# Performance work log

Measured on AMD Instinct MI355X. Metric: run time of the kernel, lower is better.

The kernel has to match this reference:

```python
import jax, jax.numpy as jnp
import numpy as np

B, S, D, H, T, MAXLEN = 8, 1024, 768, 12, 384, 1024
HD = D // H  # spatial head dim = 64
SCALE = HD ** -0.5


def setup_inputs() -> dict:
    key = jax.random.key(0)
    ks = jax.random.split(key, 16)

    def lin(k, din, dout):
        kw, _ = jax.random.split(k)
        w = jax.random.normal(kw, (din, dout), jnp.float32) / np.sqrt(din).astype(np.float32)
        b = jnp.zeros((dout,), jnp.float32)
        return w, b

    Wqs, bqs = lin(ks[0], D, D)
    Wks, bks = lin(ks[1], D, D)
    Wvs, bvs = lin(ks[2], D, D)
    Wqt, bqt = lin(ks[3], T, D)
    Wkt, bkt = lin(ks[4], T, D)
    Wvt, bvt = lin(ks[5], T, D)
    Er = jax.random.normal(ks[6], (MAXLEN, HD), jnp.float32)
    patches = jax.random.normal(ks[7], (B, S, D), jnp.float32)
    time_emb = jax.random.normal(ks[8], (B, T), jnp.float32)
    return dict(patches=patches, time_emb=time_emb,
                Wqs=Wqs, bqs=bqs, Wks=Wks, bks=bks, Wvs=Wvs, bvs=bvs,
                Wqt=Wqt, bqt=bqt, Wkt=Wkt, bkt=bkt, Wvt=Wvt, bvt=bvt, Er=Er)


def _skew(QEr):
    # QEr: [B, H, S, S] -> pad one zero col on the left, reshape, drop first row.
    b, h, r, c = QEr.shape
    padded = jnp.pad(QEr, ((0, 0), (0, 0), (0, 0), (1, 0)))  # [B,H,r,c+1]
    reshaped = padded.reshape(b, h, c + 1, r)
    return reshaped[:, :, 1:, :]  # [B,H,S,S]


def reference(patches, time_emb, Wqs, bqs, Wks, bks, Wvs, bvs,
              Wqt, bqt, Wkt, bkt, Wvt, bvt, Er):
    b, s, _ = patches.shape

    def heads(x):  # [B,S,D] -> [B,H,S,HD]
        return x.reshape(b, -1, H, HD).transpose(0, 2, 1, 3)

    qs = heads(patches @ Wqs + bqs)
    ks = heads(patches @ Wks + bks)
    vs = heads(patches @ Wvs + bvs)
    qt = heads(time_emb @ Wqt + bqt)  # [B,H,1,HD]
    kt = heads(time_emb @ Wkt + bkt)
    vt = heads(time_emb @ Wvt + bvt)

    q = qs + qt
    k = ks + kt
    v = vs + vt

    Er_slice = Er[MAXLEN - s:, :]                      # [S, HD]
    QEr = jnp.einsum('bhsd,td->bhst', qs, Er_slice)    # [B,H,S,S]
    Srel = _skew(QEr)

    scores = (jnp.einsum('bhqd,bhkd->bhqk', q, k) + Srel) * SCALE
    attn = jax.nn.softmax(scores, axis=-1)
    out = jnp.einsum('bhqk,bhkd->bhqd', attn, v)       # [B,H,S,HD]
    return out.transpose(0, 2, 1, 3).reshape(b, s, H * HD)
```

## Files before the change

kernel.cpp:

```cpp
#include <hip/hip_runtime.h>

typedef __attribute__((ext_vector_type(8))) short short8;
typedef __attribute__((ext_vector_type(4))) float floatx4;

#define CSC 0.1803368801f

__device__ __forceinline__ unsigned short f2b(float f){
  unsigned int u = __builtin_bit_cast(unsigned int, f);
  unsigned int r = (u + 0x7fffu + ((u >> 16) & 1u)) >> 16;
  return (unsigned short)r;
}
__device__ __forceinline__ float b2f(unsigned short h){
  unsigned int u = ((unsigned int)h) << 16;
  return __builtin_bit_cast(float, u);
}
__device__ __forceinline__ floatx4 mfma16(short8 a, short8 b, floatx4 c){
  return __builtin_amdgcn_mfma_f32_16x16x32_bf16(a, b, c, 0, 0, 0);
}

__global__ __launch_bounds__(256) void transpose_w(
    const float* __restrict__ Wq, const float* __restrict__ Wk,
    const float* __restrict__ Wv, unsigned short* __restrict__ Wb){
  __shared__ float tile[64][65];
  int g = blockIdx.z;
  const float* W = (g==0) ? Wq : (g==1) ? Wk : Wv;
  int r0 = blockIdx.y*64, c0 = blockIdx.x*64;
  int tx = threadIdx.x & 63, ty = threadIdx.x >> 6;
  #pragma unroll
  for (int i=0;i<16;i++){
    int r = i*4 + ty;
    tile[r][tx] = W[(r0+r)*768 + c0 + tx];
  }
  __syncthreads();
  unsigned short* dst = Wb + g*589824;
  #pragma unroll
  for (int i=0;i<16;i++){
    int rr = i*4 + ty;
    dst[(c0+rr)*768 + r0 + tx] = f2b(tile[tx][rr]);
  }
}

__global__ __launch_bounds__(256) void convert_kernel(
    const float* __restrict__ patches, const float* __restrict__ Er,
    const float* __restrict__ temb,
    const float* __restrict__ Wqt, const float* __restrict__ bqt,
    const float* __restrict__ Wkt, const float* __restrict__ bkt,
    const float* __restrict__ Wvt, const float* __restrict__ bvt,
    unsigned short* __restrict__ Pb, unsigned short* __restrict__ Erb,
    float* __restrict__ Tmat){
  int blk = blockIdx.x, tid = threadIdx.x;
  if (blk < 3104){
    const float* src; unsigned short* dst; int idx;
    if (blk < 3072){ idx = blk*2048 + tid*8; src = patches; dst = Pb; }
    else           { idx = (blk-3072)*2048 + tid*8; src = Er; dst = Erb; }
    float4 f0 = *(const float4*)(src + idx);
    float4 f1 = *(const float4*)(src + idx + 4);
    uint4 pk;
    pk.x = (unsigned)f2b(f0.x) | ((unsigned)f2b(f0.y)<<16);
    pk.y = (unsigned)f2b(f0.z) | ((unsigned)f2b(f0.w)<<16);
    pk.z = (unsigned)f2b(f1.x) | ((unsigned)f2b(f1.y)<<16);
    pk.w = (unsigned)f2b(f1.z) | ((unsigned)f2b(f1.w)<<16);
    *(uint4*)(dst + idx) = pk;
  } else {
    int g = (blk-3104)>>3, bb = (blk-3104)&7;
    const float* Wt = (g==0)? Wqt : (g==1)? Wkt : Wvt;
    const float* bt = (g==0)? bqt : (g==1)? bkt : bvt;
    __shared__ float emb[384];
    for (int j=tid;j<384;j+=256) emb[j] = temb[bb*384 + j];
    __syncthreads();
    float acc0 = bt[tid], acc1 = bt[tid+256], acc2 = bt[tid+512];
    for (int t=0;t<384;t++){
      float e = emb[t];
      const float* wr = Wt + t*768;
      acc0 += e*wr[tid]; acc1 += e*wr[tid+256]; acc2 += e*wr[tid+512];
    }
    float* dst = Tmat + g*6144 + bb*768;
    float s = (g==0) ? CSC : 1.0f;
    dst[tid] = acc0*s; dst[tid+256] = acc1*s; dst[tid+512] = acc2*s;
  }
}

__global__ __launch_bounds__(256) void qkv_gemm(
    const unsigned short* __restrict__ Pb, const unsigned short* __restrict__ Wb,
    const float* __restrict__ bq, const float* __restrict__ bk,
    const float* __restrict__ bv, const float* __restrict__ Tmat,
    unsigned short* __restrict__ Qs, unsigned short* __restrict__ K,
    unsigned short* __restrict__ V){
  __shared__ unsigned short a_lds[128*72];
  __shared__ unsigned short b_lds[128*72];
  int g = blockIdx.z;
  int m0 = blockIdx.x*128, n0 = blockIdx.y*128;
  int tid = threadIdx.x, w = tid>>6, lane = tid&63, quad = lane>>4, l16 = lane&15;
  int wr = w>>1, wc = w&1;
  const unsigned short* Wg = Wb + g*589824;
  const float* bias = (g==0)? bq : (g==1)? bk : bv;
  floatx4 acc[4][4];
  #pragma unroll
  for (int i=0;i<4;i++)
    #pragma unroll
    for (int j=0;j<4;j++) acc[i][j] = (floatx4){0.f,0.f,0.f,0.f};

  for (int kt=0; kt<12; kt++){
    int k0 = kt*64;
    __syncthreads();
    #pragma unroll
    for (int i=0;i<4;i++){
      int idx = i*256 + tid;
      int r = idx >> 3, c = (idx & 7) << 3;
      *(uint4*)&a_lds[r*72 + c] = *(const uint4*)&Pb[(m0+r)*768 + k0 + c];
      *(uint4*)&b_lds[r*72 + c] = *(const uint4*)&Wg[(n0+r)*768 + k0 + c];
    }
    __syncthreads();
    #pragma unroll
    for (int ks=0; ks<2; ks++){
      short8 af[4], bf[4];
      #pragma unroll
      for (int mb=0;mb<4;mb++)
        af[mb] = *(const short8*)&a_lds[(wr*64+mb*16+l16)*72 + ks*32 + quad*8];
      #pragma unroll
      for (int nb=0;nb<4;nb++)
        bf[nb] = *(const short8*)&b_lds[(wc*64+nb*16+l16)*72 + ks*32 + quad*8];
      #pragma unroll
      for (int mb=0;mb<4;mb++)
        #pragma unroll
        for (int nb=0;nb<4;nb++)
          acc[mb][nb] = mfma16(af[mb], bf[nb], acc[mb][nb]);
    }
  }
  #pragma unroll
  for (int mb=0;mb<4;mb++)
  #pragma unroll
  for (int nb=0;nb<4;nb++)
  #pragma unroll
  for (int reg=0;reg<4;reg++){
    int m = m0 + wr*64 + mb*16 + quad*4 + reg;
    int n = n0 + wc*64 + nb*16 + l16;
    int bb = m >> 10, s = m & 1023, h = n >> 6, hd = n & 63;
    float v = acc[mb][nb][reg] + bias[n];
    int base = (bb*12 + h) << 16;
    if (g == 0){
      Qs[base + (s<<6) + hd] = f2b(v * CSC);
    } else {
      float tadd = Tmat[g*6144 + bb*768 + n];
      if (g == 1) K[base + (s<<6) + hd] = f2b(v + tadd);
      else        V[base + (hd<<10) + s] = f2b(v + tadd);
    }
  }
}

__global__ __launch_bounds__(256, 3) void attn_kernel(
    const unsigned short* __restrict__ Qsp, const unsigned short* __restrict__ Kp,
    const unsigned short* __restrict__ Vtp, const unsigned short* __restrict__ Erb,
    const float* __restrict__ Tq, float* __restrict__ out){
  __shared__ __align__(16) char smem[29696];
  unsigned short* k_lds  = (unsigned short*)smem;
  unsigned short* v_lds  = (unsigned short*)(smem + 9216);
  unsigned short* pw_all = (unsigned short*)(smem + 18432);

  int tid = threadIdx.x, w = tid>>6, lane = tid&63, quad = lane>>4, l16 = lane&15;
  unsigned short* pw = pw_all + w*1408;
  int q0 = blockIdx.x*128, h = blockIdx.y, b = blockIdx.z;
  int hb = (b*12 + h) << 16;
  const unsigned short* Qsh = Qsp + hb;
  const unsigned short* Kh  = Kp  + hb;
  const unsigned short* Vh  = Vtp + hb;
  const float* tqv = Tq + b*768 + h*64;

  int frow = w*16 + l16;
  short8 qf[2][2], qlo[2][2], qhi[2][2];
  #pragma unroll
  for (int sub=0; sub<2; sub++){
    int qrow = q0 + sub*64 + frow;
    int qrow1 = (qrow < 1023) ? qrow+1 : 1023;
    #pragma unroll
    for (int ks=0; ks<2; ks++){
      int c = ks*32 + quad*8;
      qlo[sub][ks] = *(const short8*)&Qsh[(qrow <<6) + c];
      qhi[sub][ks] = *(const short8*)&Qsh[(qrow1<<6) + c];
      float4 t0 = *(const float4*)&tqv[c];
      float4 t1 = *(const float4*)&tqv[c+4];
      short8 qq;
      qq[0]=(short)f2b(b2f((unsigned short)qlo[sub][ks][0])+t0.x);
      qq[1]=(short)f2b(b2f((unsigned short)qlo[sub][ks][1])+t0.y);
      qq[2]=(short)f2b(b2f((unsigned short)qlo[sub][ks][2])+t0.z);
      qq[3]=(short)f2b(b2f((unsigned short)qlo[sub][ks][3])+t0.w);
      qq[4]=(short)f2b(b2f((unsigned short)qlo[sub][ks][4])+t1.x);
      qq[5]=(short)f2b(b2f((unsigned short)qlo[sub][ks][5])+t1.y);
      qq[6]=(short)f2b(b2f((unsigned short)qlo[sub][ks][6])+t1.z);
      qq[7]=(short)f2b(b2f((unsigned short)qlo[sub][ks][7])+t1.w);
      qf[sub][ks] = qq;
    }
  }

  float lpart[2][4] = {{0.f,0.f,0.f,0.f},{0.f,0.f,0.f,0.f}};
  floatx4 o_acc[2][4];
  #pragma unroll
  for (int sub=0;sub<2;sub++)
    #pragma unroll
    for (int ob=0;ob<4;ob++) o_acc[sub][ob] = (floatx4){0.f,0.f,0.f,0.f};

  int ql = quad*4;
  int ub_lo = 3 - w;

  int sr = tid>>3, scc = (tid&7)<<3;
  uint4 kr0, kr1, vr0, vr1;
  kr0 = *(const uint4*)&Kh[(sr<<6) + scc];
  kr1 = *(const uint4*)&Kh[((sr+32)<<6) + scc];
  vr0 = *(const uint4*)&Vh[(sr<<10) + scc];
  vr1 = *(const uint4*)&Vh[((sr+32)<<10) + scc];

  for (int kt=0; kt<16; kt++){
    int k0 = kt*64;
    __syncthreads();
    *(uint4*)&k_lds[sr*72 + scc]      = kr0;
    *(uint4*)&k_lds[(sr+32)*72 + scc] = kr1;
    *(uint4*)&v_lds[sr*72 + scc]      = vr0;
    *(uint4*)&v_lds[(sr+32)*72 + scc] = vr1;
    __syncthreads();
    int k0n = (kt < 15) ? k0 + 64 : k0;
    kr0 = *(const uint4*)&Kh[((k0n+sr)<<6) + scc];
    kr1 = *(const uint4*)&Kh[((k0n+sr+32)<<6) + scc];
    vr0 = *(const uint4*)&Vh[(sr<<10) + k0n + scc];
    vr1 = *(const uint4*)&Vh[((sr+32)<<10) + k0n + scc];

    floatx4 sc[2][4];
    #pragma unroll
    for (int nb=0;nb<4;nb++){
      sc[0][nb] = (floatx4){0.f,0.f,0.f,0.f};
      sc[1][nb] = (floatx4){0.f,0.f,0.f,0.f};
      #pragma unroll
      for (int ks=0;ks<2;ks++){
        short8 kf = *(const short8*)&k_lds[(nb*16+l16)*72 + ks*32 + quad*8];
        sc[0][nb] = mfma16(qf[0][ks], kf, sc[0][nb]);
        sc[1][nb] = mfma16(qf[1][ks], kf, sc[1][nb]);
      }
    }

    #pragma unroll
    for (int sub=0; sub<2; sub++){
      int diag = k0 - q0 - sub*64;
      bool needL = (diag <= 0), needU = (diag >= 0);
      bool needSel = (diag == 0) || (diag == 64);
      for (int pass=0; pass<2; pass++){
        if ((pass==0 && !needL) || (pass==1 && !needU)) continue;
        int tbase = (pass==0) ? (960 + diag) : (diag - 65);
        const short8* af = (pass==0) ? qlo[sub] : qhi[sub];
        #pragma unroll
        for (int lb=0; lb<5; lb++){
          int ub = ub_lo + lb;
          int t = tbase + ub*16 + l16;
          t = (t < 0) ? 0 : (t > 1023 ? 1023 : t);
          floatx4 pa = (floatx4){0.f,0.f,0.f,0.f};
          #pragma unroll
          for (int ks=0;ks<2;ks++){
            short8 ef = *(const short8*)&Erb[(t<<6) + ks*32 + quad*8];
            pa = mfma16(af[ks], ef, pa);
          }
          #pragma unroll
          for (int reg=0;reg<4;reg++)
            pw[(ql + reg)*88 + lb*16 + l16] = f2b(pa[reg]);
        }
        #pragma unroll
        for (int nb=0;nb<4;nb++)
        #pragma unroll
        for (int reg=0;reg<4;reg++){
          int qlr = ql + reg;
          int ki = nb*16 + l16;
          float bv = b2f(pw[qlr*88 + 15 + ki - qlr]);
          if (needSel){
            int kq = diag + ki - (w*16 + qlr);
            bool sel = (pass==0) ? (kq <= 0) : (kq >= 2);
            bv = sel ? bv : 0.f;
          }
          sc[sub][nb][reg] += bv;
        }
      }
      #pragma unroll
      for (int nb=0;nb<4;nb++)
      #pragma unroll
      for (int reg=0;reg<4;reg++){
        float p = __builtin_amdgcn_exp2f(sc[sub][nb][reg]);
        lpart[sub][reg] += p;
        pw[(ql + reg)*88 + nb*16 + l16] = f2b(p);
      }
      short8 pf[2];
      #pragma unroll
      for (int ks=0;ks<2;ks++)
        pf[ks] = *(const short8*)&pw[l16*88 + ks*32 + quad*8];
      #pragma unroll
      for (int ob=0;ob<4;ob++){
        #pragma unroll
        for (int ks=0;ks<2;ks++){
          short8 vf = *(const short8*)&v_lds[(ob*16+l16)*72 + ks*32 + quad*8];
          o_acc[sub][ob] = mfma16(pf[ks], vf, o_acc[sub][ob]);
        }
      }
    }
  }
  #pragma unroll
  for (int sub=0;sub<2;sub++){
    float rl[4];
    #pragma unroll
    for (int reg=0;reg<4;reg++){
      float l = lpart[sub][reg];
      #pragma unroll
      for (int off=1; off<16; off<<=1) l += __shfl_xor(l, off);
      rl[reg] = __builtin_amdgcn_rcpf(l);
    }
    #pragma unroll
    for (int ob=0;ob<4;ob++)
    #pragma unroll
    for (int reg=0;reg<4;reg++){
      int s = q0 + sub*64 + w*16 + quad*4 + reg;
      out[((b<<10) + s)*768 + (h<<6) + ob*16 + l16] = o_acc[sub][ob][reg] * rl[reg];
    }
  }
}

extern "C" void kernel_launch(void* const* d_in, const int* in_sizes, int n_in,
                              void* d_out, int out_size, void* d_ws, size_t ws_size,
                              hipStream_t stream) {
  const float* patches  = (const float*)d_in[0];
  const float* time_emb = (const float*)d_in[1];
  const float* Wqs = (const float*)d_in[2];  const float* bqs = (const float*)d_in[3];
  const float* Wks = (const float*)d_in[4];  const float* bks = (const float*)d_in[5];
  const float* Wvs = (const float*)d_in[6];  const float* bvs = (const float*)d_in[7];
  const float* Wqt = (const float*)d_in[8];  const float* bqt = (const float*)d_in[9];
  const float* Wkt = (const float*)d_in[10]; const float* bkt = (const float*)d_in[11];
  const float* Wvt = (const float*)d_in[12]; const float* bvt = (const float*)d_in[13];
  const float* Er  = (const float*)d_in[14];

  unsigned short* Qsp  = (unsigned short*)d_ws;
  unsigned short* Kp   = Qsp + 6291456;
  unsigned short* Vp   = Kp  + 6291456;
  unsigned short* Wbp  = Vp  + 6291456;
  unsigned short* Erbp = Wbp + 1769472;
  unsigned short* Pbp  = Erbp + 65536;
  float*          Tmat = (float*)(Pbp + 6291456);

  float* out = (float*)d_out;

  hipLaunchKernelGGL(convert_kernel, dim3(3128), dim3(256), 0, stream,
                     patches, Er, time_emb, Wqt, bqt, Wkt, bkt, Wvt, bvt,
                     Pbp, Erbp, Tmat);
  hipLaunchKernelGGL(transpose_w, dim3(12,12,3), dim3(256), 0, stream,
                     Wqs, Wks, Wvs, Wbp);
  hipLaunchKernelGGL(qkv_gemm, dim3(64,6,3), dim3(256), 0, stream,
                     Pbp, Wbp, bqs, bks, bvs, Tmat, Qsp, Kp, Vp);
  hipLaunchKernelGGL(attn_kernel, dim3(8,12,8), dim3(256), 0, stream,
                     Qsp, Kp, Vp, Erbp, Tmat, out);
}
```

Measured before the change: 360.4 us.

## Coalesce V transpose store via LDS, repack band LDS layout, share V fragments

The QKV GEMM epilogue for V now stages the tile transposed in shared memory and writes 16-byte vectors to the transposed V buffer, where it previously did scattered 2-byte stores. In the attention kernel, the relative-position band scratch is laid out column-major with packed 8-byte stores. Each sub-tile's probabilities now go to a separate LDS buffer, so one V fragment load feeds the PV MFMAs of both sub-tiles. The attention kernel's LDS use grows from about 29KB to 49KB, which may lower occupancy below the 3 blocks per CU the launch bounds target.

```diff
diff --git a/kernel.cpp b/kernel.cpp
--- a/kernel.cpp
+++ b/kernel.cpp
@@ -86,8 +86,9 @@
     const float* __restrict__ bv, const float* __restrict__ Tmat,
     unsigned short* __restrict__ Qs, unsigned short* __restrict__ K,
     unsigned short* __restrict__ V){
-  __shared__ unsigned short a_lds[128*72];
-  __shared__ unsigned short b_lds[128*72];
+  __shared__ unsigned short smem_q[18432];
+  unsigned short* a_lds = smem_q;
+  unsigned short* b_lds = smem_q + 9216;
   int g = blockIdx.z;
   int m0 = blockIdx.x*128, n0 = blockIdx.y*128;
   int tid = threadIdx.x, w = tid>>6, lane = tid&63, quad = lane>>4, l16 = lane&15;
@@ -127,23 +128,49 @@
           acc[mb][nb] = mfma16(af[mb], bf[nb], acc[mb][nb]);
     }
   }
-  #pragma unroll
-  for (int mb=0;mb<4;mb++)
-  #pragma unroll
-  for (int nb=0;nb<4;nb++)
-  #pragma unroll
-  for (int reg=0;reg<4;reg++){
-    int m = m0 + wr*64 + mb*16 + quad*4 + reg;
-    int n = n0 + wc*64 + nb*16 + l16;
-    int bb = m >> 10, s = m & 1023, h = n >> 6, hd = n & 63;
-    float v = acc[mb][nb][reg] + bias[n];
-    int base = (bb*12 + h) << 16;
-    if (g == 0){
-      Qs[base + (s<<6) + hd] = f2b(v * CSC);
-    } else {
-      float tadd = Tmat[g*6144 + bb*768 + n];
-      if (g == 1) K[base + (s<<6) + hd] = f2b(v + tadd);
-      else        V[base + (hd<<10) + s] = f2b(v + tadd);
+  if (g < 2){
+    #pragma unroll
+    for (int mb=0;mb<4;mb++)
+    #pragma unroll
+    for (int nb=0;nb<4;nb++)
+    #pragma unroll
+    for (int reg=0;reg<4;reg++){
+      int m = m0 + wr*64 + mb*16 + quad*4 + reg;
+      int n = n0 + wc*64 + nb*16 + l16;
+      int bb = m >> 10, s = m & 1023, h = n >> 6, hd = n & 63;
+      float v = acc[mb][nb][reg] + bias[n];
+      int base = (bb*12 + h) << 16;
+      if (g == 0){
+        Qs[base + (s<<6) + hd] = f2b(v * CSC);
+      } else {
+        float tadd = Tmat[6144 + bb*768 + n];
+        K[base + (s<<6) + hd] = f2b(v + tadd);
+      }
+    }
+  } else {
+    __syncthreads();
+    int bb = m0 >> 10;
+    #pragma unroll
+    for (int mb=0;mb<4;mb++)
+    #pragma unroll
+    for (int nb=0;nb<4;nb++)
+    #pragma unroll
+    for (int reg=0;reg<4;reg++){
+      int ml = wr*64 + mb*16 + quad*4 + reg;
+      int nl = wc*64 + nb*16 + l16;
+      int n = n0 + nl;
+      float v = acc[mb][nb][reg] + bias[n] + Tmat[12288 + bb*768 + n];
+      smem_q[nl*136 + ml] = f2b(v);
+    }
+    __syncthreads();
+    int s0 = m0 & 1023;
+    #pragma unroll
+    for (int i=0;i<8;i++){
+      int idx = i*256 + tid;
+      int r = idx >> 4, c8 = (idx & 15) << 3;
+      int n = n0 + r, h = n >> 6, hd = n & 63;
+      int base = (bb*12 + h) << 16;
+      *(uint4*)&V[base + (hd<<10) + s0 + c8] = *(const uint4*)&smem_q[r*136 + c8];
     }
   }
 }
@@ -152,13 +179,15 @@
     const unsigned short* __restrict__ Qsp, const unsigned short* __restrict__ Kp,
     const unsigned short* __restrict__ Vtp, const unsigned short* __restrict__ Erb,
     const float* __restrict__ Tq, float* __restrict__ out){
-  __shared__ __align__(16) char smem[29696];
-  unsigned short* k_lds  = (unsigned short*)smem;
-  unsigned short* v_lds  = (unsigned short*)(smem + 9216);
-  unsigned short* pw_all = (unsigned short*)(smem + 18432);
+  __shared__ __align__(16) char smem[49664];
+  unsigned short* k_lds = (unsigned short*)smem;
+  unsigned short* v_lds = (unsigned short*)(smem + 9216);
+  unsigned short* wbase = (unsigned short*)(smem + 18432);
 
   int tid = threadIdx.x, w = tid>>6, lane = tid&63, quad = lane>>4, l16 = lane&15;
-  unsigned short* pw = pw_all + w*1408;
+  unsigned short* bandw = wbase + w*3904;
+  unsigned short* p_l0  = bandw + 1600;
+  unsigned short* p_l1  = bandw + 2752;
   int q0 = blockIdx.x*128, h = blockIdx.y, b = blockIdx.z;
   int hb = (b*12 + h) << 16;
   const unsigned short* Qsh = Qsp + hb;
@@ -256,9 +285,10 @@
             short8 ef = *(const short8*)&Erb[(t<<6) + ks*32 + quad*8];
             pa = mfma16(af[ks], ef, pa);
           }
-          #pragma unroll
-          for (int reg=0;reg<4;reg++)
-            pw[(ql + reg)*88 + lb*16 + l16] = f2b(pa[reg]);
+          uint2 pk;
+          pk.x = (unsigned)f2b(pa[0]) | ((unsigned)f2b(pa[1])<<16);
+          pk.y = (unsigned)f2b(pa[2]) | ((unsigned)f2b(pa[3])<<16);
+          *(uint2*)&bandw[(lb*16 + l16)*20 + ql] = pk;
         }
         #pragma unroll
         for (int nb=0;nb<4;nb++)
@@ -266,7 +296,7 @@
         for (int reg=0;reg<4;reg++){
           int qlr = ql + reg;
           int ki = nb*16 + l16;
-          float bv = b2f(pw[qlr*88 + 15 + ki - qlr]);
+          float bv = b2f(bandw[(15 + ki - qlr)*20 + qlr]);
           if (needSel){
             int kq = diag + ki - (w*16 + qlr);
             bool sel = (pass==0) ? (kq <= 0) : (kq >= 2);
@@ -275,25 +305,29 @@
           sc[sub][nb][reg] += bv;
         }
       }
+      unsigned short* p_lds = (sub==0) ? p_l0 : p_l1;
       #pragma unroll
       for (int nb=0;nb<4;nb++)
       #pragma unroll
       for (int reg=0;reg<4;reg++){
         float p = __builtin_amdgcn_exp2f(sc[sub][nb][reg]);
         lpart[sub][reg] += p;
-        pw[(ql + reg)*88 + nb*16 + l16] = f2b(p);
-      }
-      short8 pf[2];
-      #pragma unroll
-      for (int ks=0;ks<2;ks++)
-        pf[ks] = *(const short8*)&pw[l16*88 + ks*32 + quad*8];
-      #pragma unroll
-      for (int ob=0;ob<4;ob++){
-        #pragma unroll
-        for (int ks=0;ks<2;ks++){
-          short8 vf = *(const short8*)&v_lds[(ob*16+l16)*72 + ks*32 + quad*8];
-          o_acc[sub][ob] = mfma16(pf[ks], vf, o_acc[sub][ob]);
-        }
+        p_lds[(ql + reg)*72 + nb*16 + l16] = f2b(p);
+      }
+    }
+    short8 pf0[2], pf1[2];
+    #pragma unroll
+    for (int ks=0;ks<2;ks++){
+      pf0[ks] = *(const short8*)&p_l0[l16*72 + ks*32 + quad*8];
+      pf1[ks] = *(const short8*)&p_l1[l16*72 + ks*32 + quad*8];
+    }
+    #pragma unroll
+    for (int ob=0;ob<4;ob++){
+      #pragma unroll
+      for (int ks=0;ks<2;ks++){
+        short8 vf = *(const short8*)&v_lds[(ob*16+l16)*72 + ks*32 + quad*8];
+        o_acc[0][ob] = mfma16(pf0[ks], vf, o_acc[0][ob]);
+        o_acc[1][ob] = mfma16(pf1[ks], vf, o_acc[1][ob]);
       }
     }
   }
```

Result: slower. 436.2 us (+21.0%).
